# Kernel tuning notes

Measured on AMD Instinct MI355X. Metric: run time of the kernel, lower is better.

The kernel has to match this reference:

```python
import jax, jax.numpy as jnp
import numpy as np

N_NODES = 100000
N_EDGES = 1600000
D_IN = 64
D_HID = 64
NEG_SLOPE = 0.01  # torch.nn.LeakyReLU default


def gcn_conv(x, W, b, src, dst, n_nodes):
    h = x @ W  # [N, F_out]
    deg = jnp.zeros((n_nodes,), x.dtype).at[dst].add(jnp.ones((src.shape[0],), x.dtype)) + 1.0
    dinv_sqrt = jax.lax.rsqrt(deg)
    norm = dinv_sqrt[src] * dinv_sqrt[dst]  # [E]
    agg = jnp.zeros_like(h).at[dst].add(norm[:, None] * h[src])
    agg = agg + h * (1.0 / deg)[:, None]  # self-loop contribution: deg^-1/2_i * deg^-1/2_i
    return agg + b


def leaky_relu(v):
    return jnp.where(v >= 0, v, NEG_SLOPE * v)


def setup_inputs() -> dict:
    key = jax.random.key(0)
    ks = jax.random.split(key, 8)
    x = jax.random.normal(ks[0], (N_NODES, D_IN), dtype=jnp.float32)
    edge_index = jax.random.randint(ks[1], (2, N_EDGES), 0, N_NODES, dtype=jnp.int32)
    s = 0.05
    W1 = jax.random.normal(ks[2], (D_IN, D_HID), dtype=jnp.float32) * s
    b1 = jnp.zeros((D_HID,), jnp.float32)
    W2 = jax.random.normal(ks[3], (D_HID, D_HID), dtype=jnp.float32) * s
    b2 = jnp.zeros((D_HID,), jnp.float32)
    W3 = jax.random.normal(ks[4], (D_HID, D_HID), dtype=jnp.float32) * s
    b3 = jnp.zeros((D_HID,), jnp.float32)
    return {"x": x, "W1": W1, "b1": b1, "W2": W2, "b2": b2, "W3": W3, "b3": b3,
            "edge_index": edge_index}


def reference(x, W1, b1, W2, b2, W3, b3, edge_index):
    src, dst = edge_index[0], edge_index[1]
    n = x.shape[0]
    # layer 1: conv -> LeakyReLU -> dropout (identity in eval / reference)
    h = leaky_relu(gcn_conv(x, W1, b1, src, dst, n))
    # layer 2: checkpoint(conv2, ...) -> plain conv, no activation
    h = gcn_conv(h, W2, b2, src, dst, n)
    # layer 3: conv -> LeakyReLU
    h = leaky_relu(gcn_conv(h, W3, b3, src, dst, n))
    return h
```

## Files before the change

### kernel.cpp

```cpp
#include <hip/hip_runtime.h>
#include <hip/hip_fp16.h>
#include <math.h>


constexpr int SHIFT = 8;
constexpr int CHUNK = 4096;
constexpr int BCAP  = 5120;

typedef _Float16 half8 __attribute__((ext_vector_type(8)));
typedef float floatx4 __attribute__((ext_vector_type(4)));

__global__ void k_hist(const int* __restrict__ dst, int E, int NB,
                       int* __restrict__ Bh) {
    __shared__ int h[512];
    int tid = threadIdx.x;
    for (int i = tid; i < 512; i += 256) h[i] = 0;
    __syncthreads();
    int s = blockIdx.x * CHUNK;
    int e = min(s + CHUNK, E);
    for (int i = s + tid; i < e; i += 256) atomicAdd(&h[dst[i] >> SHIFT], 1);
    __syncthreads();
    for (int i = tid; i < NB; i += 256) Bh[(size_t)blockIdx.x * NB + i] = h[i];
}

__global__ void k_bucket_scan(int* __restrict__ Bh, int B1, int NB,
                              int* __restrict__ total) {
    __shared__ int sh[256];
    int b = blockIdx.x;
    int tid = threadIdx.x;
    int carry = 0;
    for (int j0 = 0; j0 < B1; j0 += 256) {
        int j = j0 + tid;
        int v = (j < B1) ? Bh[(size_t)j * NB + b] : 0;
        sh[tid] = v;
        __syncthreads();
        for (int off = 1; off < 256; off <<= 1) {
            int add = (tid >= off) ? sh[tid - off] : 0;
            __syncthreads();
            sh[tid] += add;
            __syncthreads();
        }
        int excl = sh[tid] - v + carry;
        if (j < B1) Bh[(size_t)j * NB + b] = excl;
        int tot = sh[255];
        __syncthreads();
        carry += tot;
    }
    if (tid == 0) total[b] = carry;
}

__global__ void k_base_scan(const int* __restrict__ total, int NB, int E,
                            int* __restrict__ base) {
    __shared__ int sh[512];
    int tid = threadIdx.x;
    int v = (tid < NB) ? total[tid] : 0;
    sh[tid] = v;
    __syncthreads();
    for (int off = 1; off < 512; off <<= 1) {
        int add = (tid >= off) ? sh[tid - off] : 0;
        __syncthreads();
        sh[tid] += add;
        __syncthreads();
    }
    if (tid < NB) base[tid] = sh[tid] - v;
    if (tid == 0) base[NB] = E;
}

__global__ void k_scatter(const int* __restrict__ src, const int* __restrict__ dst,
                          int E, int NB, const int* __restrict__ Bh,
                          const int* __restrict__ base, unsigned* __restrict__ ebuf) {
    __shared__ int h[512];
    __shared__ int cur[512];
    __shared__ int gb[512];
    __shared__ int sh[256];
    __shared__ unsigned srec[CHUNK];
    __shared__ int spos[CHUNK];
    int tid = threadIdx.x;
    for (int i = tid; i < 512; i += 256) h[i] = 0;
    __syncthreads();
    int s = blockIdx.x * CHUNK;
    int e = min(s + CHUNK, E);
    for (int i = s + tid; i < e; i += 256) atomicAdd(&h[dst[i] >> SHIFT], 1);
    __syncthreads();
    int carry = 0;
    for (int part = 0; part < 2; part++) {
        int idx = part * 256 + tid;
        int v = h[idx];
        sh[tid] = v;
        __syncthreads();
        for (int off = 1; off < 256; off <<= 1) {
            int add = (tid >= off) ? sh[tid - off] : 0;
            __syncthreads();
            sh[tid] += add;
            __syncthreads();
        }
        int excl = sh[tid] - v + carry;
        int tot = sh[255];
        __syncthreads();
        h[idx] = excl;
        carry += tot;
        __syncthreads();
    }
    for (int b = tid; b < NB; b += 256) {
        cur[b] = h[b];
        gb[b]  = base[b] + Bh[(size_t)blockIdx.x * NB + b] - h[b];
    }
    __syncthreads();
    for (int i = s + tid; i < e; i += 256) {
        int d = dst[i];
        int b = d >> SHIFT;
        unsigned rec = ((unsigned)(d & 255) << 24) | (unsigned)src[i];
        int lpos = atomicAdd(&cur[b], 1);
        srec[lpos] = rec;
        spos[lpos] = gb[b] + lpos;
    }
    __syncthreads();
    int cntE = e - s;
    for (int t = tid; t < cntE; t += 256) ebuf[spos[t]] = srec[t];
}

__global__ void k_bucket_sort(const unsigned* __restrict__ ebuf,
                              const int* __restrict__ base, int n, int E,
                              int* __restrict__ row_ptr, int* __restrict__ col) {
    __shared__ int cnt[256];
    __shared__ int sh[256];
    __shared__ int cur[256];
    __shared__ unsigned srec[BCAP];
    int b = blockIdx.x;
    int tid = threadIdx.x;
    int s = base[b];
    int e = base[b + 1];
    int len = e - s;
    cnt[tid] = 0;
    __syncthreads();
    for (int i = s + tid; i < e; i += 256) atomicAdd(&cnt[ebuf[i] >> 24], 1);
    __syncthreads();
    int c = cnt[tid];
    sh[tid] = c;
    __syncthreads();
    for (int off = 1; off < 256; off <<= 1) {
        int add = (tid >= off) ? sh[tid - off] : 0;
        __syncthreads();
        sh[tid] += add;
        __syncthreads();
    }
    int excl = sh[tid] - c;
    int node = (b << SHIFT) | tid;
    if (node < n) row_ptr[node] = s + excl;
    cur[tid] = excl;
    __syncthreads();
    if (len <= BCAP) {
        for (int i = s + tid; i < e; i += 256) {
            unsigned v = ebuf[i];
            int lpos = atomicAdd(&cur[v >> 24], 1);
            srec[lpos] = (v & 0x00FFFFFFu) << 7;
        }
        __syncthreads();
        for (int t = tid; t < len; t += 256) col[s + t] = (int)srec[t];
    } else {
        for (int i = s + tid; i < e; i += 256) {
            unsigned v = ebuf[i];
            int lpos = atomicAdd(&cur[v >> 24], 1);
            col[s + lpos] = (int)((v & 0x00FFFFFFu) << 7);
        }
    }
    if (b == 0 && tid == 0) row_ptr[n] = E;
}

__global__ void k_gemm_scale(const float* __restrict__ X, const float* __restrict__ W,
                             const int* __restrict__ row_ptr, int n,
                             __half* __restrict__ HS) {
    __shared__ float Ws[64][64];
    __shared__ float Xs[16][68];
    int tid = threadIdx.x;
    {
        const float4* W4 = (const float4*)W;
        float4* Ws4 = (float4*)&Ws[0][0];
#pragma unroll
        for (int j = 0; j < 4; j++) Ws4[tid + 256 * j] = W4[tid + 256 * j];
    }
    int row0 = blockIdx.x * 16;
    int r = tid >> 4;
    int c4 = (tid & 15) * 4;
    {
        int grow = row0 + r;
        float4 xv = make_float4(0.f, 0.f, 0.f, 0.f);
        if (grow < n) xv = *(const float4*)&X[(size_t)grow * 64 + c4];
        *(float4*)&Xs[r][c4] = xv;
    }
    __syncthreads();

    float4 acc = make_float4(0.f, 0.f, 0.f, 0.f);
#pragma unroll
    for (int k = 0; k < 64; k++) {
        float xv = Xs[r][k];
        float4 wv = *(const float4*)&Ws[k][c4];
        acc.x += xv * wv.x;
        acc.y += xv * wv.y;
        acc.z += xv * wv.z;
        acc.w += xv * wv.w;
    }
    int grow = row0 + r;
    if (grow < n) {
        float deg = 1.0f + (float)(row_ptr[grow + 1] - row_ptr[grow]);
        float dinv = rsqrtf(deg);
        __half2 h0 = __floats2half2_rn(acc.x * dinv, acc.y * dinv);
        __half2 h1 = __floats2half2_rn(acc.z * dinv, acc.w * dinv);
        uint2 pack;
        pack.x = *(const unsigned int*)&h0;
        pack.y = *(const unsigned int*)&h1;
        *(uint2*)&HS[(size_t)grow * 64 + c4] = pack;
    }
}

__device__ inline float4 cvt_h4(uint2 v) {
    float2 f0 = __half22float2(*(__half2*)&v.x);
    float2 f1 = __half22float2(*(__half2*)&v.y);
    return make_float4(f0.x, f0.y, f1.x, f1.y);
}

__device__ inline uint2 ld_row(const char* HSb, int boff, int c) {
    return *(const uint2*)(HSb + boff + (c << 3));
}

__device__ inline float4 agg_row(const char* __restrict__ HSb,
                                 const int* __restrict__ col,
                                 int gid, int c, int r0, int r1) {
    float4 a0 = cvt_h4(*(const uint2*)(HSb + ((size_t)gid << 7) + (c << 3)));
    float4 a1 = make_float4(0.f, 0.f, 0.f, 0.f);
    float4 a2 = a1, a3 = a1;
    int e = r0;
    for (; e + 8 <= r1; e += 8) {
        int s0 = col[e + 0], s1 = col[e + 1], s2 = col[e + 2], s3 = col[e + 3];
        int s4 = col[e + 4], s5 = col[e + 5], s6 = col[e + 6], s7 = col[e + 7];
        uint2 v0 = ld_row(HSb, s0, c), v1 = ld_row(HSb, s1, c);
        uint2 v2 = ld_row(HSb, s2, c), v3 = ld_row(HSb, s3, c);
        uint2 v4 = ld_row(HSb, s4, c), v5 = ld_row(HSb, s5, c);
        uint2 v6 = ld_row(HSb, s6, c), v7 = ld_row(HSb, s7, c);
        float4 f0 = cvt_h4(v0), f1 = cvt_h4(v1), f2 = cvt_h4(v2), f3 = cvt_h4(v3);
        float4 f4 = cvt_h4(v4), f5 = cvt_h4(v5), f6 = cvt_h4(v6), f7 = cvt_h4(v7);
        a0.x += f0.x; a0.y += f0.y; a0.z += f0.z; a0.w += f0.w;
        a1.x += f1.x; a1.y += f1.y; a1.z += f1.z; a1.w += f1.w;
        a2.x += f2.x; a2.y += f2.y; a2.z += f2.z; a2.w += f2.w;
        a3.x += f3.x; a3.y += f3.y; a3.z += f3.z; a3.w += f3.w;
        a0.x += f4.x; a0.y += f4.y; a0.z += f4.z; a0.w += f4.w;
        a1.x += f5.x; a1.y += f5.y; a1.z += f5.z; a1.w += f5.w;
        a2.x += f6.x; a2.y += f6.y; a2.z += f6.z; a2.w += f6.w;
        a3.x += f7.x; a3.y += f7.y; a3.z += f7.z; a3.w += f7.w;
    }
    if (e + 4 <= r1) {
        int s0 = col[e + 0], s1 = col[e + 1], s2 = col[e + 2], s3 = col[e + 3];
        uint2 v0 = ld_row(HSb, s0, c), v1 = ld_row(HSb, s1, c);
        uint2 v2 = ld_row(HSb, s2, c), v3 = ld_row(HSb, s3, c);
        float4 f0 = cvt_h4(v0), f1 = cvt_h4(v1), f2 = cvt_h4(v2), f3 = cvt_h4(v3);
        a0.x += f0.x; a0.y += f0.y; a0.z += f0.z; a0.w += f0.w;
        a1.x += f1.x; a1.y += f1.y; a1.z += f1.z; a1.w += f1.w;
        a2.x += f2.x; a2.y += f2.y; a2.z += f2.z; a2.w += f2.w;
        a3.x += f3.x; a3.y += f3.y; a3.z += f3.z; a3.w += f3.w;
        e += 4;
    }
    if (e + 0 < r1) {
        float4 f = cvt_h4(ld_row(HSb, col[e + 0], c));
        a0.x += f.x; a0.y += f.y; a0.z += f.z; a0.w += f.w;
    }
    if (e + 1 < r1) {
        float4 f = cvt_h4(ld_row(HSb, col[e + 1], c));
        a1.x += f.x; a1.y += f.y; a1.z += f.z; a1.w += f.w;
    }
    if (e + 2 < r1) {
        float4 f = cvt_h4(ld_row(HSb, col[e + 2], c));
        a2.x += f.x; a2.y += f.y; a2.z += f.z; a2.w += f.w;
    }
    float4 s;
    s.x = (a0.x + a1.x) + (a2.x + a3.x);
    s.y = (a0.y + a1.y) + (a2.y + a3.y);
    s.z = (a0.z + a1.z) + (a2.z + a3.z);
    s.w = (a0.w + a1.w) + (a2.w + a3.w);
    return s;
}

template <bool RELU>
__global__ void k_agg_gemm(const __half* __restrict__ HS, const int* __restrict__ row_ptr,
                           const int* __restrict__ col, const float* __restrict__ bias,
                           const float* __restrict__ Wn, int n,
                           __half* __restrict__ HSn) {
    __shared__ _Float16 WtS[64 * 72];
    __shared__ _Float16 rowS[16 * 72];
    __shared__ float dinvS[16];
    int tid = threadIdx.x;

    {
        const float4* W4 = (const float4*)Wn;
#pragma unroll
        for (int j = 0; j < 4; j++) {
            int idx = tid + 256 * j;
            int row = idx >> 4;
            int col0 = (idx & 15) * 4;
            float4 wv = W4[idx];
            WtS[(col0 + 0) * 72 + row] = (_Float16)wv.x;
            WtS[(col0 + 1) * 72 + row] = (_Float16)wv.y;
            WtS[(col0 + 2) * 72 + row] = (_Float16)wv.z;
            WtS[(col0 + 3) * 72 + row] = (_Float16)wv.w;
        }
    }

    int g = tid >> 4;
    int c = tid & 15;
    int gid = blockIdx.x * 16 + g;
    bool valid = gid < n;

    float dinv = 1.0f;
    if (valid) {
        const char* __restrict__ HSb = (const char*)HS;
        int r0 = row_ptr[gid];
        int r1 = row_ptr[gid + 1];
        float4 s = agg_row(HSb, col, gid, c, r0, r1);
        float deg = 1.0f + (float)(r1 - r0);
        dinv = rsqrtf(deg);
        float4 bv = *(const float4*)&bias[4 * c];
        float vx = dinv * s.x + bv.x;
        float vy = dinv * s.y + bv.y;
        float vz = dinv * s.z + bv.z;
        float vw = dinv * s.w + bv.w;
        if (RELU) {
            vx = (vx >= 0.f) ? vx : 0.01f * vx;
            vy = (vy >= 0.f) ? vy : 0.01f * vy;
            vz = (vz >= 0.f) ? vz : 0.01f * vz;
            vw = (vw >= 0.f) ? vw : 0.01f * vw;
        }
        __half2 h0 = __floats2half2_rn(vx, vy);
        __half2 h1 = __floats2half2_rn(vz, vw);
        uint2 pack;
        pack.x = *(const unsigned int*)&h0;
        pack.y = *(const unsigned int*)&h1;
        *(uint2*)&rowS[g * 72 + c * 4] = pack;
        if (c == 0) dinvS[g] = dinv;
    }
    __syncthreads();

    int w = tid >> 6;
    int lane = tid & 63;
    int ar = lane & 15;
    int ks = lane >> 4;

    half8 a1 = *(const half8*)&rowS[ar * 72 + ks * 8];
    half8 a2 = *(const half8*)&rowS[ar * 72 + 32 + ks * 8];
    half8 b1 = *(const half8*)&WtS[(w * 16 + ar) * 72 + ks * 8];
    half8 b2 = *(const half8*)&WtS[(w * 16 + ar) * 72 + 32 + ks * 8];

    floatx4 acc = {0.f, 0.f, 0.f, 0.f};
    acc = __builtin_amdgcn_mfma_f32_16x16x32_f16(a1, b1, acc, 0, 0, 0);
    acc = __builtin_amdgcn_mfma_f32_16x16x32_f16(a2, b2, acc, 0, 0, 0);

    int node0 = (lane >> 4) * 4;
    float4 dv4 = *(const float4*)&dinvS[node0];
    int colg = w * 16 + (lane & 15);
    int base_node = blockIdx.x * 16 + node0;
#pragma unroll
    for (int reg = 0; reg < 4; reg++) {
        int node_g = base_node + reg;
        if (node_g < n) {
            float dv = (reg == 0) ? dv4.x : (reg == 1) ? dv4.y : (reg == 2) ? dv4.z : dv4.w;
            HSn[(size_t)node_g * 64 + colg] = __float2half(acc[reg] * dv);
        }
    }
}

__global__ void k_agg_out(const __half* __restrict__ HS, const int* __restrict__ row_ptr,
                          const int* __restrict__ col, const float* __restrict__ bias,
                          int n, float* __restrict__ out) {
    int gid = (int)((blockIdx.x * (unsigned)blockDim.x + threadIdx.x) >> 4);
    if (gid >= n) return;
    int c = threadIdx.x & 15;
    const char* __restrict__ HSb = (const char*)HS;
    int r0 = row_ptr[gid];
    int r1 = row_ptr[gid + 1];
    float4 s = agg_row(HSb, col, gid, c, r0, r1);
    float deg = 1.0f + (float)(r1 - r0);
    float dinv = rsqrtf(deg);
    float4 bv = *(const float4*)&bias[4 * c];
    float vx = dinv * s.x + bv.x;
    float vy = dinv * s.y + bv.y;
    float vz = dinv * s.z + bv.z;
    float vw = dinv * s.w + bv.w;
    vx = (vx >= 0.f) ? vx : 0.01f * vx;
    vy = (vy >= 0.f) ? vy : 0.01f * vy;
    vz = (vz >= 0.f) ? vz : 0.01f * vz;
    vw = (vw >= 0.f) ? vw : 0.01f * vw;
    *(float4*)&out[(size_t)gid * 64 + 4 * c] = make_float4(vx, vy, vz, vw);
}

static inline size_t align256(size_t x) { return (x + 255) & ~(size_t)255; }

extern "C" void kernel_launch(void* const* d_in, const int* in_sizes, int n_in,
                              void* d_out, int out_size, void* d_ws, size_t ws_size,
                              hipStream_t stream) {
    const float* x  = (const float*)d_in[0];
    const float* W1 = (const float*)d_in[1];
    const float* b1 = (const float*)d_in[2];
    const float* W2 = (const float*)d_in[3];
    const float* b2 = (const float*)d_in[4];
    const float* W3 = (const float*)d_in[5];
    const float* b3 = (const float*)d_in[6];
    const int* edge = (const int*)d_in[7];

    int n = in_sizes[0] / 64;
    int E = in_sizes[7] / 2;
    const int* srcp = edge;
    const int* dstp = edge + E;

    int NB = (n + 255) >> SHIFT;
    int B1 = (E + CHUNK - 1) / CHUNK;

    char* ws = (char*)d_ws;
    int* row_ptr   = (int*)ws;      ws += align256((size_t)(n + 1) * 4);
    int* Bh        = (int*)ws;      ws += align256((size_t)B1 * NB * 4);
    int* total     = (int*)ws;      ws += align256((size_t)NB * 4);
    int* base      = (int*)ws;      ws += align256((size_t)(NB + 1) * 4);
    unsigned* ebuf = (unsigned*)ws; ws += align256((size_t)E * 4);
    int* col       = (int*)ws;      ws += align256((size_t)E * 4);
    __half* hs_a   = (__half*)ws;   ws += align256((size_t)n * 64 * 2);
    __half* hs_b   = (__half*)ws;   ws += align256((size_t)n * 64 * 2);
    float* out     = (float*)d_out;

    k_hist<<<B1, 256, 0, stream>>>(dstp, E, NB, Bh);
    k_bucket_scan<<<NB, 256, 0, stream>>>(Bh, B1, NB, total);
    k_base_scan<<<1, 512, 0, stream>>>(total, NB, E, base);
    k_scatter<<<B1, 256, 0, stream>>>(srcp, dstp, E, NB, Bh, base, ebuf);
    k_bucket_sort<<<NB, 256, 0, stream>>>(ebuf, base, n, E, row_ptr, col);

    int blocks16 = (n + 15) / 16;

    k_gemm_scale<<<blocks16, 256, 0, stream>>>(x, W1, row_ptr, n, hs_a);
    k_agg_gemm<true><<<blocks16, 256, 0, stream>>>(hs_a, row_ptr, col, b1, W2, n, hs_b);
    k_agg_gemm<false><<<blocks16, 256, 0, stream>>>(hs_b, row_ptr, col, b2, W3, n, hs_a);
    k_agg_out<<<blocks16, 256, 0, stream>>>(hs_a, row_ptr, col, b3, n, out);
}
```

Before: 170.7 us.

## Use wave-shuffle scans, reuse histogram counts, cache bucket edges, MFMA first GEMM

Replaces the LDS Hillis-Steele block scans with a wave-shuffle scan helper, which cuts the number of barriers. The scatter kernel now reads a saved copy of the per-chunk histogram instead of re-reading dst and recounting. The bucket sort stages its edges in shared memory so ebuf is read from global once. The first layer's GEMM moves from fp32 FMA to fp16 MFMA through shared helpers, which adds an extra workspace array and rounds x to fp16 before the multiply.

```diff
diff --git a/kernel.cpp b/kernel.cpp
--- a/kernel.cpp
+++ b/kernel.cpp
@@ -10,8 +10,25 @@
 typedef _Float16 half8 __attribute__((ext_vector_type(8)));
 typedef float floatx4 __attribute__((ext_vector_type(4)));
 
+__device__ inline int scan256(int v, int tid, int* wsum, int* total) {
+    int lane = tid & 63, w = tid >> 6;
+    int inc = v;
+#pragma unroll
+    for (int off = 1; off < 64; off <<= 1) {
+        int t = __shfl_up(inc, off);
+        if (lane >= off) inc += t;
+    }
+    if (lane == 63) wsum[w] = inc;
+    __syncthreads();
+    int s0 = wsum[0], s1 = wsum[1], s2 = wsum[2], s3 = wsum[3];
+    __syncthreads();
+    int base = (w > 0 ? s0 : 0) + (w > 1 ? s1 : 0) + (w > 2 ? s2 : 0);
+    *total = s0 + s1 + s2 + s3;
+    return base + (inc - v);
+}
+
 __global__ void k_hist(const int* __restrict__ dst, int E, int NB,
-                       int* __restrict__ Bh) {
+                       int* __restrict__ Bh, int* __restrict__ Bc) {
     __shared__ int h[512];
     int tid = threadIdx.x;
     for (int i = tid; i < 512; i += 256) h[i] = 0;
@@ -20,30 +37,25 @@
     int e = min(s + CHUNK, E);
     for (int i = s + tid; i < e; i += 256) atomicAdd(&h[dst[i] >> SHIFT], 1);
     __syncthreads();
-    for (int i = tid; i < NB; i += 256) Bh[(size_t)blockIdx.x * NB + i] = h[i];
+    for (int i = tid; i < NB; i += 256) {
+        int v = h[i];
+        Bh[(size_t)blockIdx.x * NB + i] = v;
+        Bc[(size_t)blockIdx.x * NB + i] = v;
+    }
 }
 
 __global__ void k_bucket_scan(int* __restrict__ Bh, int B1, int NB,
                               int* __restrict__ total) {
-    __shared__ int sh[256];
+    __shared__ int wsum[4];
     int b = blockIdx.x;
     int tid = threadIdx.x;
     int carry = 0;
     for (int j0 = 0; j0 < B1; j0 += 256) {
         int j = j0 + tid;
         int v = (j < B1) ? Bh[(size_t)j * NB + b] : 0;
-        sh[tid] = v;
-        __syncthreads();
-        for (int off = 1; off < 256; off <<= 1) {
-            int add = (tid >= off) ? sh[tid - off] : 0;
-            __syncthreads();
-            sh[tid] += add;
-            __syncthreads();
-        }
-        int excl = sh[tid] - v + carry;
-        if (j < B1) Bh[(size_t)j * NB + b] = excl;
-        int tot = sh[255];
-        __syncthreads();
+        int tot;
+        int ex = scan256(v, tid, wsum, &tot);
+        if (j < B1) Bh[(size_t)j * NB + b] = ex + carry;
         carry += tot;
     }
     if (tid == 0) total[b] = carry;
@@ -51,61 +63,48 @@
 
 __global__ void k_base_scan(const int* __restrict__ total, int NB, int E,
                             int* __restrict__ base) {
-    __shared__ int sh[512];
-    int tid = threadIdx.x;
-    int v = (tid < NB) ? total[tid] : 0;
-    sh[tid] = v;
-    __syncthreads();
-    for (int off = 1; off < 512; off <<= 1) {
-        int add = (tid >= off) ? sh[tid - off] : 0;
-        __syncthreads();
-        sh[tid] += add;
-        __syncthreads();
-    }
-    if (tid < NB) base[tid] = sh[tid] - v;
+    __shared__ int wsum[4];
+    int tid = threadIdx.x;
+    int b0 = 2 * tid, b1 = 2 * tid + 1;
+    int v0 = (b0 < NB) ? total[b0] : 0;
+    int v1 = (b1 < NB) ? total[b1] : 0;
+    int tot;
+    int ex = scan256(v0 + v1, tid, wsum, &tot);
+    if (b0 < NB) base[b0] = ex;
+    if (b1 < NB) base[b1] = ex + v0;
     if (tid == 0) base[NB] = E;
 }
 
 __global__ void k_scatter(const int* __restrict__ src, const int* __restrict__ dst,
                           int E, int NB, const int* __restrict__ Bh,
-                          const int* __restrict__ base, unsigned* __restrict__ ebuf) {
-    __shared__ int h[512];
+                          const int* __restrict__ Bc, const int* __restrict__ base,
+                          unsigned* __restrict__ ebuf) {
     __shared__ int cur[512];
     __shared__ int gb[512];
-    __shared__ int sh[256];
+    __shared__ int wsum[4];
     __shared__ unsigned srec[CHUNK];
     __shared__ int spos[CHUNK];
     int tid = threadIdx.x;
-    for (int i = tid; i < 512; i += 256) h[i] = 0;
-    __syncthreads();
-    int s = blockIdx.x * CHUNK;
+    int j = blockIdx.x;
+
+    int b0 = 2 * tid, b1 = 2 * tid + 1;
+    int c0 = (b0 < NB) ? Bc[(size_t)j * NB + b0] : 0;
+    int c1 = (b1 < NB) ? Bc[(size_t)j * NB + b1] : 0;
+    int tot;
+    int ex = scan256(c0 + c1, tid, wsum, &tot);
+    if (b0 < NB) {
+        cur[b0] = ex;
+        gb[b0]  = base[b0] + Bh[(size_t)j * NB + b0] - ex;
+    }
+    if (b1 < NB) {
+        int ex1 = ex + c0;
+        cur[b1] = ex1;
+        gb[b1]  = base[b1] + Bh[(size_t)j * NB + b1] - ex1;
+    }
+    __syncthreads();
+
+    int s = j * CHUNK;
     int e = min(s + CHUNK, E);
-    for (int i = s + tid; i < e; i += 256) atomicAdd(&h[dst[i] >> SHIFT], 1);
-    __syncthreads();
-    int carry = 0;
-    for (int part = 0; part < 2; part++) {
-        int idx = part * 256 + tid;
-        int v = h[idx];
-        sh[tid] = v;
-        __syncthreads();
-        for (int off = 1; off < 256; off <<= 1) {
-            int add = (tid >= off) ? sh[tid - off] : 0;
-            __syncthreads();
-            sh[tid] += add;
-            __syncthreads();
-        }
-        int excl = sh[tid] - v + carry;
-        int tot = sh[255];
-        __syncthreads();
-        h[idx] = excl;
-        carry += tot;
-        __syncthreads();
-    }
-    for (int b = tid; b < NB; b += 256) {
-        cur[b] = h[b];
-        gb[b]  = base[b] + Bh[(size_t)blockIdx.x * NB + b] - h[b];
-    }
-    __syncthreads();
     for (int i = s + tid; i < e; i += 256) {
         int d = dst[i];
         int b = d >> SHIFT;
@@ -123,9 +122,10 @@
                               const int* __restrict__ base, int n, int E,
                               int* __restrict__ row_ptr, int* __restrict__ col) {
     __shared__ int cnt[256];
-    __shared__ int sh[256];
     __shared__ int cur[256];
-    __shared__ unsigned srec[BCAP];
+    __shared__ int wsum[4];
+    __shared__ unsigned raw[BCAP];
+    __shared__ int sorted[BCAP];
     int b = blockIdx.x;
     int tid = threadIdx.x;
     int s = base[b];
@@ -133,31 +133,35 @@
     int len = e - s;
     cnt[tid] = 0;
     __syncthreads();
-    for (int i = s + tid; i < e; i += 256) atomicAdd(&cnt[ebuf[i] >> 24], 1);
-    __syncthreads();
-    int c = cnt[tid];
-    sh[tid] = c;
-    __syncthreads();
-    for (int off = 1; off < 256; off <<= 1) {
-        int add = (tid >= off) ? sh[tid - off] : 0;
-        __syncthreads();
-        sh[tid] += add;
-        __syncthreads();
-    }
-    int excl = sh[tid] - c;
-    int node = (b << SHIFT) | tid;
-    if (node < n) row_ptr[node] = s + excl;
-    cur[tid] = excl;
-    __syncthreads();
     if (len <= BCAP) {
-        for (int i = s + tid; i < e; i += 256) {
-            unsigned v = ebuf[i];
-            int lpos = atomicAdd(&cur[v >> 24], 1);
-            srec[lpos] = (v & 0x00FFFFFFu) << 7;
+        for (int t = tid; t < len; t += 256) {
+            unsigned v = ebuf[s + t];
+            raw[t] = v;
+            atomicAdd(&cnt[v >> 24], 1);
         }
         __syncthreads();
-        for (int t = tid; t < len; t += 256) col[s + t] = (int)srec[t];
+        int tot;
+        int ex = scan256(cnt[tid], tid, wsum, &tot);
+        int node = (b << SHIFT) | tid;
+        if (node < n) row_ptr[node] = s + ex;
+        cur[tid] = ex;
+        __syncthreads();
+        for (int t = tid; t < len; t += 256) {
+            unsigned v = raw[t];
+            int lpos = atomicAdd(&cur[v >> 24], 1);
+            sorted[lpos] = (int)((v & 0x00FFFFFFu) << 7);
+        }
+        __syncthreads();
+        for (int t = tid; t < len; t += 256) col[s + t] = sorted[t];
     } else {
+        for (int i = s + tid; i < e; i += 256) atomicAdd(&cnt[ebuf[i] >> 24], 1);
+        __syncthreads();
+        int tot;
+        int ex = scan256(cnt[tid], tid, wsum, &tot);
+        int node = (b << SHIFT) | tid;
+        if (node < n) row_ptr[node] = s + ex;
+        cur[tid] = ex;
+        __syncthreads();
         for (int i = s + tid; i < e; i += 256) {
             unsigned v = ebuf[i];
             int lpos = atomicAdd(&cur[v >> 24], 1);
@@ -167,50 +171,77 @@
     if (b == 0 && tid == 0) row_ptr[n] = E;
 }
 
+__device__ inline void mfma_rows_store(const _Float16* rowS, const _Float16* WtS,
+                                       const float* dinvS, int n, int blockRow0,
+                                       int tid, __half* __restrict__ HSn) {
+    int w = tid >> 6;
+    int lane = tid & 63;
+    int ar = lane & 15;
+    int ks = lane >> 4;
+
+    half8 a1 = *(const half8*)&rowS[ar * 72 + ks * 8];
+    half8 a2 = *(const half8*)&rowS[ar * 72 + 32 + ks * 8];
+    half8 b1 = *(const half8*)&WtS[(w * 16 + ar) * 72 + ks * 8];
+    half8 b2 = *(const half8*)&WtS[(w * 16 + ar) * 72 + 32 + ks * 8];
+
+    floatx4 acc = {0.f, 0.f, 0.f, 0.f};
+    acc = __builtin_amdgcn_mfma_f32_16x16x32_f16(a1, b1, acc, 0, 0, 0);
+    acc = __builtin_amdgcn_mfma_f32_16x16x32_f16(a2, b2, acc, 0, 0, 0);
+
+    int node0 = (lane >> 4) * 4;
+    float4 dv4 = *(const float4*)&dinvS[node0];
+    int colg = w * 16 + (lane & 15);
+    int base_node = blockRow0 + node0;
+#pragma unroll
+    for (int reg = 0; reg < 4; reg++) {
+        int node_g = base_node + reg;
+        if (node_g < n) {
+            float dv = (reg == 0) ? dv4.x : (reg == 1) ? dv4.y : (reg == 2) ? dv4.z : dv4.w;
+            HSn[(size_t)node_g * 64 + colg] = __float2half(acc[reg] * dv);
+        }
+    }
+}
+
+__device__ inline void stage_wt(const float* __restrict__ Wn, _Float16* WtS, int tid) {
+    const float4* W4 = (const float4*)Wn;
+#pragma unroll
+    for (int j = 0; j < 4; j++) {
+        int idx = tid + 256 * j;
+        int row = idx >> 4;
+        int col0 = (idx & 15) * 4;
+        float4 wv = W4[idx];
+        WtS[(col0 + 0) * 72 + row] = (_Float16)wv.x;
+        WtS[(col0 + 1) * 72 + row] = (_Float16)wv.y;
+        WtS[(col0 + 2) * 72 + row] = (_Float16)wv.z;
+        WtS[(col0 + 3) * 72 + row] = (_Float16)wv.w;
+    }
+}
+
 __global__ void k_gemm_scale(const float* __restrict__ X, const float* __restrict__ W,
                              const int* __restrict__ row_ptr, int n,
                              __half* __restrict__ HS) {
-    __shared__ float Ws[64][64];
-    __shared__ float Xs[16][68];
-    int tid = threadIdx.x;
-    {
-        const float4* W4 = (const float4*)W;
-        float4* Ws4 = (float4*)&Ws[0][0];
-#pragma unroll
-        for (int j = 0; j < 4; j++) Ws4[tid + 256 * j] = W4[tid + 256 * j];
-    }
-    int row0 = blockIdx.x * 16;
-    int r = tid >> 4;
-    int c4 = (tid & 15) * 4;
-    {
-        int grow = row0 + r;
-        float4 xv = make_float4(0.f, 0.f, 0.f, 0.f);
-        if (grow < n) xv = *(const float4*)&X[(size_t)grow * 64 + c4];
-        *(float4*)&Xs[r][c4] = xv;
-    }
-    __syncthreads();
-
-    float4 acc = make_float4(0.f, 0.f, 0.f, 0.f);
-#pragma unroll
-    for (int k = 0; k < 64; k++) {
-        float xv = Xs[r][k];
-        float4 wv = *(const float4*)&Ws[k][c4];
-        acc.x += xv * wv.x;
-        acc.y += xv * wv.y;
-        acc.z += xv * wv.z;
-        acc.w += xv * wv.w;
-    }
-    int grow = row0 + r;
-    if (grow < n) {
-        float deg = 1.0f + (float)(row_ptr[grow + 1] - row_ptr[grow]);
-        float dinv = rsqrtf(deg);
-        __half2 h0 = __floats2half2_rn(acc.x * dinv, acc.y * dinv);
-        __half2 h1 = __floats2half2_rn(acc.z * dinv, acc.w * dinv);
+    __shared__ _Float16 WtS[64 * 72];
+    __shared__ _Float16 rowS[16 * 72];
+    __shared__ float dinvS[16];
+    int tid = threadIdx.x;
+    stage_wt(W, WtS, tid);
+
+    int g = tid >> 4;
+    int c = tid & 15;
+    int gid = blockIdx.x * 16 + g;
+    if (gid < n) {
+        float4 xv = *(const float4*)&X[(size_t)gid * 64 + c * 4];
+        __half2 h0 = __floats2half2_rn(xv.x, xv.y);
+        __half2 h1 = __floats2half2_rn(xv.z, xv.w);
         uint2 pack;
         pack.x = *(const unsigned int*)&h0;
         pack.y = *(const unsigned int*)&h1;
-        *(uint2*)&HS[(size_t)grow * 64 + c4] = pack;
-    }
+        *(uint2*)&rowS[g * 72 + c * 4] = pack;
+        if (c == 0)
+            dinvS[g] = rsqrtf(1.0f + (float)(row_ptr[gid + 1] - row_ptr[gid]));
+    }
+    __syncthreads();
+    mfma_rows_store(rowS, WtS, dinvS, n, blockIdx.x * 16, tid, HS);
 }
 
 __device__ inline float4 cvt_h4(uint2 v) {
@@ -288,35 +319,19 @@
     __shared__ _Float16 rowS[16 * 72];
     __shared__ float dinvS[16];
     int tid = threadIdx.x;
-
-    {
-        const float4* W4 = (const float4*)Wn;
-#pragma unroll
-        for (int j = 0; j < 4; j++) {
-            int idx = tid + 256 * j;
-            int row = idx >> 4;
-            int col0 = (idx & 15) * 4;
-            float4 wv = W4[idx];
-            WtS[(col0 + 0) * 72 + row] = (_Float16)wv.x;
-            WtS[(col0 + 1) * 72 + row] = (_Float16)wv.y;
-            WtS[(col0 + 2) * 72 + row] = (_Float16)wv.z;
-            WtS[(col0 + 3) * 72 + row] = (_Float16)wv.w;
-        }
-    }
+    stage_wt(Wn, WtS, tid);
 
     int g = tid >> 4;
     int c = tid & 15;
     int gid = blockIdx.x * 16 + g;
-    bool valid = gid < n;
-
-    float dinv = 1.0f;
-    if (valid) {
+
+    if (gid < n) {
         const char* __restrict__ HSb = (const char*)HS;
         int r0 = row_ptr[gid];
         int r1 = row_ptr[gid + 1];
         float4 s = agg_row(HSb, col, gid, c, r0, r1);
         float deg = 1.0f + (float)(r1 - r0);
-        dinv = rsqrtf(deg);
+        float dinv = rsqrtf(deg);
         float4 bv = *(const float4*)&bias[4 * c];
         float vx = dinv * s.x + bv.x;
         float vy = dinv * s.y + bv.y;
@@ -337,33 +352,7 @@
         if (c == 0) dinvS[g] = dinv;
     }
     __syncthreads();
-
-    int w = tid >> 6;
-    int lane = tid & 63;
-    int ar = lane & 15;
-    int ks = lane >> 4;
-
-    half8 a1 = *(const half8*)&rowS[ar * 72 + ks * 8];
-    half8 a2 = *(const half8*)&rowS[ar * 72 + 32 + ks * 8];
-    half8 b1 = *(const half8*)&WtS[(w * 16 + ar) * 72 + ks * 8];
-    half8 b2 = *(const half8*)&WtS[(w * 16 + ar) * 72 + 32 + ks * 8];
-
-    floatx4 acc = {0.f, 0.f, 0.f, 0.f};
-    acc = __builtin_amdgcn_mfma_f32_16x16x32_f16(a1, b1, acc, 0, 0, 0);
-    acc = __builtin_amdgcn_mfma_f32_16x16x32_f16(a2, b2, acc, 0, 0, 0);
-
-    int node0 = (lane >> 4) * 4;
-    float4 dv4 = *(const float4*)&dinvS[node0];
-    int colg = w * 16 + (lane & 15);
-    int base_node = blockIdx.x * 16 + node0;
-#pragma unroll
-    for (int reg = 0; reg < 4; reg++) {
-        int node_g = base_node + reg;
-        if (node_g < n) {
-            float dv = (reg == 0) ? dv4.x : (reg == 1) ? dv4.y : (reg == 2) ? dv4.z : dv4.w;
-            HSn[(size_t)node_g * 64 + colg] = __float2half(acc[reg] * dv);
-        }
-    }
+    mfma_rows_store(rowS, WtS, dinvS, n, blockIdx.x * 16, tid, HSn);
 }
 
 __global__ void k_agg_out(const __half* __restrict__ HS, const int* __restrict__ row_ptr,
@@ -415,6 +404,7 @@
     char* ws = (char*)d_ws;
     int* row_ptr   = (int*)ws;      ws += align256((size_t)(n + 1) * 4);
     int* Bh        = (int*)ws;      ws += align256((size_t)B1 * NB * 4);
+    int* Bc        = (int*)ws;      ws += align256((size_t)B1 * NB * 4);
     int* total     = (int*)ws;      ws += align256((size_t)NB * 4);
     int* base      = (int*)ws;      ws += align256((size_t)(NB + 1) * 4);
     unsigned* ebuf = (unsigned*)ws; ws += align256((size_t)E * 4);
@@ -423,10 +413,10 @@
     __half* hs_b   = (__half*)ws;   ws += align256((size_t)n * 64 * 2);
     float* out     = (float*)d_out;
 
-    k_hist<<<B1, 256, 0, stream>>>(dstp, E, NB, Bh);
+    k_hist<<<B1, 256, 0, stream>>>(dstp, E, NB, Bh, Bc);
     k_bucket_scan<<<NB, 256, 0, stream>>>(Bh, B1, NB, total);
-    k_base_scan<<<1, 512, 0, stream>>>(total, NB, E, base);
-    k_scatter<<<B1, 256, 0, stream>>>(srcp, dstp, E, NB, Bh, base, ebuf);
+    k_base_scan<<<1, 256, 0, stream>>>(total, NB, E, base);
+    k_scatter<<<B1, 256, 0, stream>>>(srcp, dstp, E, NB, Bh, Bc, base, ebuf);
     k_bucket_sort<<<NB, 256, 0, stream>>>(ebuf, base, n, E, row_ptr, col);
 
     int blocks16 = (n + 15) / 16;
```

Result: faster. 160.4 us (-6.0%).
